# Kernel optimization log

Hardware: AMD Instinct MI355X
Metric: run time of the kernel (lower is better)

## Reference

```python
import jax, jax.numpy as jnp
import numpy as np

B, S, D, H = 4, 2048, 256, 4
HD = D // H          # head_dim = 64
SPARSITY = 0.1
NH2 = H * H          # 16, distill feature size


def _linear_params(key, out_d, in_d):
    # torch nn.Linear default init: U(-1/sqrt(in), 1/sqrt(in)) for W and b
    limit = 1.0 / np.sqrt(in_d)
    kw, kb = jax.random.split(key)
    W = jax.random.uniform(kw, (out_d, in_d), minval=-limit, maxval=limit, dtype=jnp.float32)
    b = jax.random.uniform(kb, (out_d,), minval=-limit, maxval=limit, dtype=jnp.float32)
    return W, b


def setup_inputs() -> dict:
    key = jax.random.key(0)
    ks = jax.random.split(key, 8)
    x = jax.random.normal(ks[0], (B, S, D), dtype=jnp.float32)
    Wq, bq = _linear_params(ks[1], D, D)
    Wk, bk = _linear_params(ks[2], D, D)
    Wv, bv = _linear_params(ks[3], D, D)
    Wd, bd = _linear_params(ks[4], NH2, NH2)      # distill: 16 -> 16
    Wg, bg = _linear_params(ks[5], NH2, D)        # gate: dim -> 16 (then sigmoid)
    Wgp, bgp = _linear_params(ks[6], D, NH2)      # gate_projection: 16 -> dim
    Wo, bo = _linear_params(ks[7], D, D)          # out: dim -> dim
    return dict(x=x, Wq=Wq, bq=bq, Wk=Wk, bk=bk, Wv=Wv, bv=bv,
                Wd=Wd, bd=bd, Wg=Wg, bg=bg, Wgp=Wgp, bgp=bgp, Wo=Wo, bo=bo)


def reference(x, Wq, bq, Wk, bk, Wv, bv, Wd, bd, Wg, bg, Wgp, bgp, Wo, bo):
    b, s, d = x.shape
    scale = HD ** -0.5
    # QKV projections, split into heads: [b, h, s, hd]
    Q = (x @ Wq.T + bq).reshape(b, s, H, HD).transpose(0, 2, 1, 3)
    K = (x @ Wk.T + bk).reshape(b, s, H, HD).transpose(0, 2, 1, 3)
    V = (x @ Wv.T + bv).reshape(b, s, H, HD).transpose(0, 2, 1, 3)
    scores = jnp.einsum('bhqd,bhkd->bhqk', Q, K) * scale  # [b,h,s,s]
    # per-row quantile threshold (torch.quantile linear interpolation == jnp default)
    q = 1.0 - SPARSITY  # 0.9
    thr = jnp.quantile(scores, q, axis=-1, keepdims=True)
    masked = jnp.where(scores >= thr, scores, -jnp.inf)
    probs = jax.nn.softmax(masked, axis=-1)
    att = jnp.einsum('bhqk,bhkd->bhqd', probs, V)
    att = att.transpose(0, 2, 1, 3).reshape(b, s, d)  # [b,s,dim]
    # distill: view as (-1, 16) -> Linear(16,16) -> view back
    distilled = (att.reshape(-1, NH2) @ Wd.T + bd).reshape(b, s, d)
    # gate from mean-pooled input
    g = jax.nn.sigmoid(x.mean(axis=1) @ Wg.T + bg)  # [b,16]
    g = (g @ Wgp.T + bgp)[:, None, :]               # [b,1,dim] broadcast over seq
    mixed = g * distilled + (1.0 - g) * att
    return mixed @ Wo.T + bo
```

## Files before the change

### kernel.cpp

```cpp
#include <hip/hip_runtime.h>
#include <hip/hip_bf16.h>
#include <math.h>


#define CAP 128

typedef __attribute__((ext_vector_type(8))) short short8;
typedef __attribute__((ext_vector_type(4))) float floatx4;
typedef _Float16 half8 __attribute__((ext_vector_type(8)));
typedef _Float16 half4v __attribute__((ext_vector_type(4)));
#define MFMA16(a,b,c) __builtin_amdgcn_mfma_f32_16x16x32_bf16(a,b,c,0,0,0)
#define MFMAH(a,b,c)  __builtin_amdgcn_mfma_f32_16x16x32_f16(a,b,c,0,0,0)

__device__ __forceinline__ float umt(unsigned u){
  return __uint_as_float((u & 0x80000000u) ? (u & 0x7fffffffu) : ~u);
}
__device__ __forceinline__ float wmin_f(float v){
  #pragma unroll
  for (int m=1;m<64;m<<=1) v = fminf(v, __shfl_xor(v,m,64));
  return v;
}
__device__ __forceinline__ int mbcnt64(unsigned long long m){
  return (int)__builtin_amdgcn_mbcnt_hi((unsigned)(m>>32),
         __builtin_amdgcn_mbcnt_lo((unsigned)(m & 0xffffffffull), 0u));
}
__device__ __forceinline__ short8 ldb8(const __hip_bfloat16* p){
  return *(const short8*)p;
}

#define FULLSEL(SU, PSTART, V206, V205)                                        \
  {                                                                            \
    unsigned v = (PSTART);                                                     \
    _Pragma("unroll 1")                                                        \
    for (int bit = 19; bit >= 0; --bit){                                       \
      const float cf = umt(v | (1u << bit));                                   \
      int n = 0;                                                               \
      _Pragma("unroll")                                                        \
      for (int i = 0; i < 32; i++) n += (int)__popcll(__ballot(SU[i] >= cf));  \
      if (n >= 206) v |= (1u << bit);                                          \
    }                                                                          \
    V206 = umt(v);                                                             \
    int cgt = 0; float mn = 3.0e38f;                                           \
    _Pragma("unroll")                                                          \
    for (int i = 0; i < 32; i++){                                              \
      const float u = SU[i];                                                   \
      const bool gt = (u > V206);                                              \
      cgt += (int)__popcll(__ballot(gt));                                      \
      mn = (gt && u < mn) ? u : mn;                                            \
    }                                                                          \
    mn = wmin_f(mn);                                                           \
    V205 = (cgt == 205) ? mn : V206;                                           \
  }

__global__ void xpart_kernel(const float* __restrict__ x, float* __restrict__ xpart){
  const int ch = blockIdx.x, b = blockIdx.y, t = threadIdx.x;
  const float* xp = x + ((size_t)b*2048 + (size_t)ch*128)*256 + t;
  float s = 0.f;
  for (int i=0;i<128;i++) s += xp[(size_t)i*256];
  xpart[(size_t)(b*16+ch)*256 + t] = s;
}

__global__ void gate_kernel(const float* __restrict__ xpart,
                            const float* __restrict__ Wg, const float* __restrict__ bg,
                            const float* __restrict__ Wgp,const float* __restrict__ bgp,
                            float* __restrict__ gate_ws){
  __shared__ float xm[256];
  __shared__ float g16[16];
  const int t = threadIdx.x;
  const int b = blockIdx.x;
  float s = 0.f;
  for (int ch=0; ch<16; ch++) s += xpart[(size_t)(b*16+ch)*256 + t];
  xm[t] = s * (1.0f/2048.0f);
  __syncthreads();
  if (t < 16){
    float z = bg[t];
    for (int d=0; d<256; d++) z = fmaf(xm[d], Wg[t*256+d], z);
    g16[t] = 1.0f/(1.0f + __expf(-z));
  }
  __syncthreads();
  float z2 = bgp[t];
  #pragma unroll
  for (int j=0;j<16;j++) z2 = fmaf(g16[j], Wgp[t*16+j], z2);
  gate_ws[b*256 + t] = z2;
}

__global__ __launch_bounds__(256) void qkv_gemm(
    const float* __restrict__ x,
    const float* __restrict__ Wq, const float* __restrict__ bq,
    const float* __restrict__ Wk, const float* __restrict__ bk,
    const float* __restrict__ Wv, const float* __restrict__ bv,
    __hip_bfloat16* __restrict__ qh, __hip_bfloat16* __restrict__ ql,
    __hip_bfloat16* __restrict__ kh, __hip_bfloat16* __restrict__ kl,
    _Float16* __restrict__ vth, _Float16* __restrict__ vtl){
  __shared__ float As[16][68];
  __shared__ float Bs[16][68];
  const int m0 = blockIdx.x * 64;
  const int n0g = blockIdx.y * 64;
  const int sect = n0g >> 8;
  const int nloc0 = n0g & 255;
  const float* W    = (sect==0) ? Wq : ((sect==1) ? Wk : Wv);
  const float* bias = (sect==0) ? bq : ((sect==1) ? bk : bv);
  const int tid = threadIdx.x;
  const int ty = tid >> 4, tx = tid & 15;
  const int lr = tid >> 2, lc = tid & 3;

  float c[4][4];
  #pragma unroll
  for (int i=0;i<4;i++){
    #pragma unroll
    for (int j=0;j<4;j++) c[i][j]=0.f;
  }

  for (int k0=0; k0<256; k0+=16){
    float4 av  = *(const float4*)&x[(size_t)(m0+lr)*256 + k0 + lc*4];
    float4 bv4 = *(const float4*)&W[(size_t)(nloc0+lr)*256 + k0 + lc*4];
    __syncthreads();
    As[lc*4+0][lr]=av.x;  As[lc*4+1][lr]=av.y;  As[lc*4+2][lr]=av.z;  As[lc*4+3][lr]=av.w;
    Bs[lc*4+0][lr]=bv4.x; Bs[lc*4+1][lr]=bv4.y; Bs[lc*4+2][lr]=bv4.z; Bs[lc*4+3][lr]=bv4.w;
    __syncthreads();
    #pragma unroll
    for (int kk=0; kk<16; kk++){
      float4 a  = *(const float4*)&As[kk][ty*4];
      float4 b4 = *(const float4*)&Bs[kk][tx*4];
      c[0][0]=fmaf(a.x,b4.x,c[0][0]); c[0][1]=fmaf(a.x,b4.y,c[0][1]); c[0][2]=fmaf(a.x,b4.z,c[0][2]); c[0][3]=fmaf(a.x,b4.w,c[0][3]);
      c[1][0]=fmaf(a.y,b4.x,c[1][0]); c[1][1]=fmaf(a.y,b4.y,c[1][1]); c[1][2]=fmaf(a.y,b4.z,c[1][2]); c[1][3]=fmaf(a.y,b4.w,c[1][3]);
      c[2][0]=fmaf(a.z,b4.x,c[2][0]); c[2][1]=fmaf(a.z,b4.y,c[2][1]); c[2][2]=fmaf(a.z,b4.z,c[2][2]); c[2][3]=fmaf(a.z,b4.w,c[2][3]);
      c[3][0]=fmaf(a.w,b4.x,c[3][0]); c[3][1]=fmaf(a.w,b4.y,c[3][1]); c[3][2]=fmaf(a.w,b4.z,c[3][2]); c[3][3]=fmaf(a.w,b4.w,c[3][3]);
    }
  }

  if (sect == 2){
    const int mB = m0 + ty*4;
    const int bidx = mB >> 11, s0 = mB & 2047;
    #pragma unroll
    for (int j=0;j<4;j++){
      const int f = nloc0 + tx*4 + j;
      const int hh = f >> 6, hd = f & 63;
      const float bf = bias[f];
      half4v hv, lv;
      #pragma unroll
      for (int i=0;i<4;i++){
        const float val = c[i][j] + bf;
        const _Float16 hx = (_Float16)val;
        hv[i] = hx;
        lv[i] = (_Float16)(val - (float)hx);
      }
      const size_t row = (size_t)((bidx*4+hh)*64 + hd);
      *(half4v*)(vth + row*2048 + s0) = hv;
      *(half4v*)(vtl + row*2048 + s0) = lv;
    }
  } else {
    #pragma unroll
    for (int i=0;i<4;i++){
      const int m = m0 + ty*4 + i;
      const int bidx = m >> 11, s = m & 2047;
      #pragma unroll
      for (int j=0;j<4;j++){
        const int f = nloc0 + tx*4 + j;
        const float val = c[i][j] + bias[f];
        const int hh = f >> 6, hd = f & 63;
        const size_t idx = (size_t)((bidx*4+hh)*2048 + s)*64 + hd;
        const __hip_bfloat16 hi = __float2bfloat16(val);
        const float lo = val - __bfloat162float(hi);
        if (sect == 0){ qh[idx] = hi; ql[idx] = __float2bfloat16(lo); }
        else          { kh[idx] = hi; kl[idx] = __float2bfloat16(lo); }
      }
    }
  }
}

__global__ __launch_bounds__(512, 4) void attn_kernel(
    const __hip_bfloat16* __restrict__ qh, const __hip_bfloat16* __restrict__ ql,
    const __hip_bfloat16* __restrict__ kh, const __hip_bfloat16* __restrict__ kl,
    const _Float16* __restrict__ vth, const _Float16* __restrict__ vtl,
    const float* __restrict__ Wd, const float* __restrict__ bd,
    const float* __restrict__ gate_ws, float* __restrict__ mix_ws){
  __shared__ __align__(16) char smem[74240];
  __shared__ float obuf[16][66];
  __shared__ float zbuf[16];

  float (*buf0)[516] = (float (*)[516])smem;
  float (*buf1)[516] = (float (*)[516])(smem + 33024);

  const int bh = blockIdx.y;
  const int q0 = blockIdx.x * 16;
  const int tid = threadIdx.x;
  const int w = tid >> 6, ln = tid & 63;
  const int lm = ln & 15;
  const int lk = (ln >> 4) * 8;
  const int qa = 2*w, qb = 2*w + 1;

  const __hip_bfloat16* Qh = qh + ((size_t)bh*2048 + q0)*64;
  const __hip_bfloat16* Ql = ql + ((size_t)bh*2048 + q0)*64;
  const __hip_bfloat16* Kh = kh + ((size_t)bh*2048 + w*256)*64;
  const __hip_bfloat16* Kl = kl + ((size_t)bh*2048 + w*256)*64;

  float su0[32], su1[32];

  const short8 ah0 = ldb8(Qh + lm*64 + lk);
  const short8 ah1 = ldb8(Qh + lm*64 + 32 + lk);
  const short8 al0 = ldb8(Ql + lm*64 + lk);
  const short8 al1 = ldb8(Ql + lm*64 + 32 + lk);

  #pragma unroll
  for (int c = 0; c < 4; c++){
    float (*bufc)[516] = (c & 1) ? buf1 : buf0;
    floatx4 acc[4];
    #pragma unroll
    for (int tl = 0; tl < 4; tl++){
      const int krow = c*64 + tl*16 + lm;
      short8 bh0 = ldb8(Kh + krow*64 + lk);
      short8 bh1 = ldb8(Kh + krow*64 + 32 + lk);
      short8 bl0 = ldb8(Kl + krow*64 + lk);
      short8 bl1 = ldb8(Kl + krow*64 + 32 + lk);
      floatx4 a = {0.f,0.f,0.f,0.f};
      a = MFMA16(ah0, bh0, a);
      a = MFMA16(ah1, bh1, a);
      a = MFMA16(al0, bh0, a);
      a = MFMA16(al1, bh1, a);
      a = MFMA16(ah0, bl0, a);
      a = MFMA16(ah1, bl1, a);
      a = MFMA16(al0, bl0, a);
      a = MFMA16(al1, bl1, a);
      acc[tl] = a;
    }
    const int wr = (ln >> 4) * 4;
    #pragma unroll
    for (int tl = 0; tl < 4; tl++){
      const int col = w*64 + tl*16 + lm;
      bufc[wr+0][col] = acc[tl].x * 0.125f;
      bufc[wr+1][col] = acc[tl].y * 0.125f;
      bufc[wr+2][col] = acc[tl].z * 0.125f;
      bufc[wr+3][col] = acc[tl].w * 0.125f;
    }
    __syncthreads();
    float4 ra0 = *(const float4*)&bufc[qa][4*ln];
    float4 ra1 = *(const float4*)&bufc[qa][256 + 4*ln];
    float4 rb0 = *(const float4*)&bufc[qb][4*ln];
    float4 rb1 = *(const float4*)&bufc[qb][256 + 4*ln];
    const int o = c*8;
    su0[o+0]=ra0.x; su0[o+1]=ra0.y; su0[o+2]=ra0.z; su0[o+3]=ra0.w;
    su0[o+4]=ra1.x; su0[o+5]=ra1.y; su0[o+6]=ra1.z; su0[o+7]=ra1.w;
    su1[o+0]=rb0.x; su1[o+1]=rb0.y; su1[o+2]=rb0.z; su1[o+3]=rb0.w;
    su1[o+4]=rb1.x; su1[o+5]=rb1.y; su1[o+6]=rb1.z; su1[o+7]=rb1.w;
  }
  __syncthreads();

  unsigned p0 = 0, p1 = 0;
  #pragma unroll 1
  for (int bit = 31; bit >= 20; --bit){
    const float c0f = umt(p0 | (1u << bit));
    const float c1f = umt(p1 | (1u << bit));
    int v0 = 0, n1 = 0;
    #pragma unroll
    for (int i = 0; i < 32; i++){
      v0 += (su0[i] >= c0f) ? 1 : 0;
      n1 += (int)__popcll(__ballot(su1[i] >= c1f));
    }
    #pragma unroll
    for (int m=1;m<64;m<<=1) v0 += __shfl_xor(v0,m,64);
    p0 |= (v0 >= 206) ? (1u << bit) : 0u;
    if (n1 >= 206) p1 |= (1u << bit);
  }

  const int b = bh >> 2, h = bh & 3;

  const float pf0  = umt(p0),             pf1  = umt(p1);
  const float hif0 = umt(p0 + 0x100000u), hif1 = umt(p1 + 0x100000u);
  float* cand0 = (float*)(smem + 65536 + (size_t)(2*w + 0)*512);
  float* cand1 = (float*)(smem + 65536 + (size_t)(2*w + 1)*512);

  int above0 = 0, nc0 = 0, above1 = 0, nc1 = 0;
  float mx0 = -3.0e38f, mx1 = -3.0e38f, mnab0 = 3.0e38f, mnab1 = 3.0e38f;
  #pragma unroll
  for (int i = 0; i < 32; i++){
    const float u0 = su0[i], u1 = su1[i];
    mx0 = fmaxf(mx0, u0);
    mx1 = fmaxf(mx1, u1);
    const bool ab0 = (u0 >= hif0), ab1 = (u1 >= hif1);
    above0 += ab0 ? 1 : 0;
    above1 += ab1 ? 1 : 0;
    if (ab0) mnab0 = fminf(mnab0, u0);
    if (ab1) mnab1 = fminf(mnab1, u1);
    const bool cd0 = (u0 >= pf0) && !ab0, cd1 = (u1 >= pf1) && !ab1;
    const unsigned long long bal0 = __ballot(cd0);
    if (cd0){
      const int pos = nc0 + mbcnt64(bal0);
      if (pos < CAP) cand0[pos] = u0;
    }
    nc0 += (int)__popcll(bal0);
    const unsigned long long bal1 = __ballot(cd1);
    if (cd1){
      const int pos = nc1 + mbcnt64(bal1);
      if (pos < CAP) cand1[pos] = u1;
    }
    nc1 += (int)__popcll(bal1);
  }
  int ab01 = above0 | (above1 << 16);
  #pragma unroll
  for (int m=1;m<64;m<<=1){
    ab01  += __shfl_xor(ab01, m,64);
    mx0   = fmaxf(mx0,   __shfl_xor(mx0,  m,64));
    mx1   = fmaxf(mx1,   __shfl_xor(mx1,  m,64));
    mnab0 = fminf(mnab0, __shfl_xor(mnab0,m,64));
    mnab1 = fminf(mnab1, __shfl_xor(mnab1,m,64));
  }
  above0 = ab01 & 0xffff;
  above1 = ab01 >> 16;

  float v206_0, v205_0, v206_1, v205_1;
  if (__builtin_expect(nc0 <= CAP && nc1 <= CAP, 1)){
    const int j0 = 206 - above0, j1 = 206 - above1;
    const float cv00 = (ln      < nc0) ? cand0[ln]      : -3.0e38f;
    const float cv01 = (ln + 64 < nc0) ? cand0[ln + 64] : -3.0e38f;
    const float cv10 = (ln      < nc1) ? cand1[ln]      : -3.0e38f;
    const float cv11 = (ln + 64 < nc1) ? cand1[ln + 64] : -3.0e38f;
    unsigned v0 = p0, v1 = p1;
    #pragma unroll 1
    for (int bit = 19; bit >= 0; --bit){
      const float cf0 = umt(v0 | (1u << bit));
      const float cf1 = umt(v1 | (1u << bit));
      const int n0 = (int)__popcll(__ballot(cv00 >= cf0))
                   + (int)__popcll(__ballot(cv01 >= cf0));
      const int n1 = (int)__popcll(__ballot(cv10 >= cf1))
                   + (int)__popcll(__ballot(cv11 >= cf1));
      if (n0 >= j0) v0 |= (1u << bit);
      if (n1 >= j1) v1 |= (1u << bit);
    }
    v206_0 = umt(v0);
    v206_1 = umt(v1);
    const int cgtc0 = (int)__popcll(__ballot(cv00 > v206_0))
                    + (int)__popcll(__ballot(cv01 > v206_0));
    const int cgtc1 = (int)__popcll(__ballot(cv10 > v206_1))
                    + (int)__popcll(__ballot(cv11 > v206_1));
    float mnc0 = 3.0e38f, mnc1 = 3.0e38f;
    if (cv00 > v206_0) mnc0 = fminf(mnc0, cv00);
    if (cv01 > v206_0) mnc0 = fminf(mnc0, cv01);
    if (cv10 > v206_1) mnc1 = fminf(mnc1, cv10);
    if (cv11 > v206_1) mnc1 = fminf(mnc1, cv11);
    #pragma unroll
    for (int m=1;m<64;m<<=1){
      mnc0 = fminf(mnc0, __shfl_xor(mnc0,m,64));
      mnc1 = fminf(mnc1, __shfl_xor(mnc1,m,64));
    }
    const int cgt0 = above0 + cgtc0, cgt1 = above1 + cgtc1;
    v205_0 = (cgt0 == 205) ? ((cgtc0 > 0) ? mnc0 : mnab0) : v206_0;
    v205_1 = (cgt1 == 205) ? ((cgtc1 > 0) ? mnc1 : mnab1) : v206_1;
  } else {
    FULLSEL(su0, p0, v206_0, v205_0);
    FULLSEL(su1, p1, v206_1, v205_1);
  }

  const float thr0 = (float)((double)v206_0 + 0.3*((double)v205_0 - (double)v206_0));
  const float thr1 = (float)((double)v206_1 + 0.3*((double)v205_1 - (double)v206_1));

  float zl0 = 0.f, zl1 = 0.f;
  char* rba = smem + (size_t)qa*4096 + ((size_t)(ln >> 4) << 9)
            + (size_t)((((ln & 15) << 3)) ^ ((qa & 7) << 4));
  char* rbb = smem + (size_t)qb*4096 + ((size_t)(ln >> 4) << 9)
            + (size_t)((((ln & 15) << 3)) ^ ((qb & 7) << 4));
  #pragma unroll
  for (int c = 0; c < 4; c++){
    #pragma unroll
    for (int h4 = 0; h4 < 2; h4++){
      half4v pk0, pk1;
      #pragma unroll
      for (int jj = 0; jj < 4; jj++){
        const int i = c*8 + h4*4 + jj;
        const float s0 = su0[i], s1 = su1[i];
        const float pr0 = (s0 >= thr0) ? __expf(s0 - mx0) : 0.f;
        const float pr1 = (s1 >= thr1) ? __expf(s1 - mx1) : 0.f;
        const _Float16 ph0 = (_Float16)pr0;
        const _Float16 ph1 = (_Float16)pr1;
        zl0 += (float)ph0;
        zl1 += (float)ph1;
        pk0[jj] = ph0;
        pk1[jj] = ph1;
      }
      *(half4v*)(rba + h4*2048 + c*128) = pk0;
      *(half4v*)(rbb + h4*2048 + c*128) = pk1;
    }
  }
  #pragma unroll
  for (int m=1;m<64;m<<=1){
    zl0 += __shfl_xor(zl0,m,64);
    zl1 += __shfl_xor(zl1,m,64);
  }
  if (ln == 0){ zbuf[qa] = 1.0f / zl0; zbuf[qb] = 1.0f / zl1; }

  __syncthreads();

  const int ct = w & 3, kh2 = w >> 2;
  const int arow = ln & 15;
  const int sw = (arow & 7) << 4;
  const char* prow = smem + (size_t)arow*4096;
  const int klog0 = (kh2 << 11) + ((ln >> 4) << 4);
  const _Float16* vhp = vth + ((size_t)bh*64 + ct*16 + arow)*2048 + (kh2 << 10) + ((ln >> 4) << 3);
  const _Float16* vlp = vtl + ((size_t)bh*64 + ct*16 + arow)*2048 + (kh2 << 10) + ((ln >> 4) << 3);

  floatx4 acch = {0.f,0.f,0.f,0.f};
  floatx4 accl = {0.f,0.f,0.f,0.f};
  #pragma unroll 4
  for (int kk = 0; kk < 32; kk++){
    const half8 a   = *(const half8*)(prow + ((klog0 + kk*64) ^ sw));
    const half8 vh8 = *(const half8*)(vhp + kk*32);
    const half8 vl8 = *(const half8*)(vlp + kk*32);
    acch = MFMAH(a, vh8, acch);
    accl = MFMAH(a, vl8, accl);
  }
  floatx4 acc = acch + accl;

  float gt = 0.f, bda = 0.f;
  float wdv[16];
  if (kh2 == 1){
    const int r0 = (ln >> 4) * 4;
    #pragma unroll
    for (int i = 0; i < 4; i++) obuf[r0+i][ct*16 + arow] = acc[i];
  } else {
    gt  = gate_ws[(size_t)b*256 + h*64 + ct*16 + arow];
    bda = bd[arow];
    #pragma unroll
    for (int m4 = 0; m4 < 4; m4++){
      const float4 t4 = *(const float4*)&Wd[arow*16 + m4*4];
      wdv[m4*4+0]=t4.x; wdv[m4*4+1]=t4.y; wdv[m4*4+2]=t4.z; wdv[m4*4+3]=t4.w;
    }
  }
  __syncthreads();
  if (kh2 == 0){
    const int r0 = (ln >> 4) * 4;
    const int gb = ln & 48;
    #pragma unroll
    for (int i = 0; i < 4; i++){
      const int r = r0 + i;
      const float o = (acc[i] + obuf[r][ct*16 + arow]) * zbuf[r];
      float d = bda;
      #pragma unroll
      for (int m = 0; m < 16; m++)
        d = fmaf(__shfl(o, gb + m, 64), wdv[m], d);
      const float mixed = gt*d + (1.0f - gt)*o;
      mix_ws[(size_t)(b*2048 + q0 + r)*256 + h*64 + ct*16 + arow] = mixed;
    }
  }
}

__global__ __launch_bounds__(256) void out_gemm(
    const float* __restrict__ A, const float* __restrict__ Wo,
    const float* __restrict__ bo, float* __restrict__ out){
  __shared__ float As[16][68];
  __shared__ float Bs[16][68];
  const int m0 = blockIdx.x * 64;
  const int n0 = blockIdx.y * 64;
  const int tid = threadIdx.x;
  const int ty = tid >> 4, tx = tid & 15;
  const int lr = tid >> 2, lc = tid & 3;

  float c[4][4];
  #pragma unroll
  for (int i=0;i<4;i++){
    #pragma unroll
    for (int j=0;j<4;j++) c[i][j]=0.f;
  }

  for (int k0=0; k0<256; k0+=16){
    float4 av  = *(const float4*)&A[(size_t)(m0+lr)*256 + k0 + lc*4];
    float4 bv4 = *(const float4*)&Wo[(size_t)(n0+lr)*256 + k0 + lc*4];
    __syncthreads();
    As[lc*4+0][lr]=av.x;  As[lc*4+1][lr]=av.y;  As[lc*4+2][lr]=av.z;  As[lc*4+3][lr]=av.w;
    Bs[lc*4+0][lr]=bv4.x; Bs[lc*4+1][lr]=bv4.y; Bs[lc*4+2][lr]=bv4.z; Bs[lc*4+3][lr]=bv4.w;
    __syncthreads();
    #pragma unroll
    for (int kk=0; kk<16; kk++){
      float4 a  = *(const float4*)&As[kk][ty*4];
      float4 b4 = *(const float4*)&Bs[kk][tx*4];
      c[0][0]=fmaf(a.x,b4.x,c[0][0]); c[0][1]=fmaf(a.x,b4.y,c[0][1]); c[0][2]=fmaf(a.x,b4.z,c[0][2]); c[0][3]=fmaf(a.x,b4.w,c[0][3]);
      c[1][0]=fmaf(a.y,b4.x,c[1][0]); c[1][1]=fmaf(a.y,b4.y,c[1][1]); c[1][2]=fmaf(a.y,b4.z,c[1][2]); c[1][3]=fmaf(a.y,b4.w,c[1][3]);
      c[2][0]=fmaf(a.z,b4.x,c[2][0]); c[2][1]=fmaf(a.z,b4.y,c[2][1]); c[2][2]=fmaf(a.z,b4.z,c[2][2]); c[2][3]=fmaf(a.z,b4.w,c[2][3]);
      c[3][0]=fmaf(a.w,b4.x,c[3][0]); c[3][1]=fmaf(a.w,b4.y,c[3][1]); c[3][2]=fmaf(a.w,b4.z,c[3][2]); c[3][3]=fmaf(a.w,b4.w,c[3][3]);
    }
  }
  #pragma unroll
  for (int i=0;i<4;i++){
    const int m = m0 + ty*4 + i;
    float4 st = make_float4(c[i][0]+bo[n0+tx*4+0], c[i][1]+bo[n0+tx*4+1],
                            c[i][2]+bo[n0+tx*4+2], c[i][3]+bo[n0+tx*4+3]);
    *(float4*)&out[(size_t)m*256 + n0 + tx*4] = st;
  }
}

extern "C" void kernel_launch(void* const* d_in, const int* in_sizes, int n_in,
                              void* d_out, int out_size, void* d_ws, size_t ws_size,
                              hipStream_t stream) {
  const float* x   = (const float*)d_in[0];
  const float* Wq  = (const float*)d_in[1];  const float* bq  = (const float*)d_in[2];
  const float* Wk  = (const float*)d_in[3];  const float* bk  = (const float*)d_in[4];
  const float* Wv  = (const float*)d_in[5];  const float* bv  = (const float*)d_in[6];
  const float* Wd  = (const float*)d_in[7];  const float* bd  = (const float*)d_in[8];
  const float* Wg  = (const float*)d_in[9];  const float* bg  = (const float*)d_in[10];
  const float* Wgp = (const float*)d_in[11]; const float* bgp = (const float*)d_in[12];
  const float* Wo  = (const float*)d_in[13]; const float* bo  = (const float*)d_in[14];

  char* base = (char*)d_ws;
  float* mix_ws = (float*)(base);
  __hip_bfloat16* qh = (__hip_bfloat16*)(base + (size_t)( 8<<20));
  __hip_bfloat16* ql = (__hip_bfloat16*)(base + (size_t)(12<<20));
  __hip_bfloat16* kh = (__hip_bfloat16*)(base + (size_t)(16<<20));
  __hip_bfloat16* kl = (__hip_bfloat16*)(base + (size_t)(20<<20));
  _Float16* vth = (_Float16*)(base + (size_t)(24<<20));
  _Float16* vtl = (_Float16*)(base + (size_t)(28<<20));
  float* xpart  = (float*)(base + (size_t)(32<<20));
  float* gate_ws= (float*)(base + (size_t)(32<<20) + 65536);

  xpart_kernel<<<dim3(16,4), 256, 0, stream>>>(x, xpart);
  gate_kernel<<<4, 256, 0, stream>>>(xpart, Wg, bg, Wgp, bgp, gate_ws);
  qkv_gemm<<<dim3(128,12), 256, 0, stream>>>(x, Wq,bq, Wk,bk, Wv,bv, qh,ql,kh,kl, vth,vtl);
  attn_kernel<<<dim3(128,16), 512, 0, stream>>>(qh, ql, kh, kl, vth, vtl,
                                                Wd, bd, gate_ws, mix_ws);
  out_gemm<<<dim3(128,4), 256, 0, stream>>>(mix_ws, Wo, bo, (float*)d_out);
}
```

Before: 438.8 us.

## Move QKV and output projections to split-bf16 MFMA GEMMs

Replaces the FP32 SIMT shared-memory GEMMs for the QKV and output projections with bf16 MFMA 16x16x32 kernels. They use a hi/lo split (three-term products plus lo*lo) to keep near-FP32 accuracy. Inputs x and the weight matrices are pre-split into bf16 hi/lo buffers by the xpart kernel and a new weight-conversion kernel. The attention kernel now writes its mixed output as hi/lo bf16 as well. This trades an extra launch and extra workspace traffic for matrix-core throughput in the projection GEMMs.

```diff
diff --git a/kernel.cpp b/kernel.cpp
--- a/kernel.cpp
+++ b/kernel.cpp
@@ -52,12 +52,42 @@
     V205 = (cgt == 205) ? mn : V206;                                           \
   }
 
-__global__ void xpart_kernel(const float* __restrict__ x, float* __restrict__ xpart){
+__global__ void xpart_kernel(const float* __restrict__ x, float* __restrict__ xpart,
+                             __hip_bfloat16* __restrict__ xh, __hip_bfloat16* __restrict__ xl){
   const int ch = blockIdx.x, b = blockIdx.y, t = threadIdx.x;
-  const float* xp = x + ((size_t)b*2048 + (size_t)ch*128)*256 + t;
+  const size_t base = ((size_t)b*2048 + (size_t)ch*128)*256 + t;
   float s = 0.f;
-  for (int i=0;i<128;i++) s += xp[(size_t)i*256];
+  for (int i=0;i<128;i++){
+    const float v = x[base + (size_t)i*256];
+    s += v;
+    const __hip_bfloat16 h = __float2bfloat16(v);
+    xh[base + (size_t)i*256] = h;
+    xl[base + (size_t)i*256] = __float2bfloat16(v - __bfloat162float(h));
+  }
   xpart[(size_t)(b*16+ch)*256 + t] = s;
+}
+
+__global__ void wconv_kernel(const float* __restrict__ Wq, const float* __restrict__ Wk,
+                             const float* __restrict__ Wv, const float* __restrict__ Wo,
+                             __hip_bfloat16* __restrict__ wh, __hip_bfloat16* __restrict__ wl){
+  const int mat = blockIdx.x >> 6;
+  const float* W = (mat==0) ? Wq : (mat==1) ? Wk : (mat==2) ? Wv : Wo;
+  const int off = (blockIdx.x & 63)*1024 + threadIdx.x*4;
+  const float4 v = *(const float4*)&W[off];
+  short4 h4, l4;
+  const float vv[4] = {v.x, v.y, v.z, v.w};
+  short hs[4], ls[4];
+  #pragma unroll
+  for (int i=0;i<4;i++){
+    const __hip_bfloat16 h = __float2bfloat16(vv[i]);
+    const __hip_bfloat16 l = __float2bfloat16(vv[i] - __bfloat162float(h));
+    hs[i] = *(const short*)&h; ls[i] = *(const short*)&l;
+  }
+  h4 = make_short4(hs[0],hs[1],hs[2],hs[3]);
+  l4 = make_short4(ls[0],ls[1],ls[2],ls[3]);
+  const size_t o = (size_t)mat*65536 + off;
+  *(short4*)((short*)wh + o) = h4;
+  *(short4*)((short*)wl + o) = l4;
 }
 
 __global__ void gate_kernel(const float* __restrict__ xpart,
@@ -85,62 +115,55 @@
 }
 
 __global__ __launch_bounds__(256) void qkv_gemm(
-    const float* __restrict__ x,
-    const float* __restrict__ Wq, const float* __restrict__ bq,
-    const float* __restrict__ Wk, const float* __restrict__ bk,
-    const float* __restrict__ Wv, const float* __restrict__ bv,
+    const __hip_bfloat16* __restrict__ xh, const __hip_bfloat16* __restrict__ xl,
+    const __hip_bfloat16* __restrict__ wh, const __hip_bfloat16* __restrict__ wl,
+    const float* __restrict__ bq, const float* __restrict__ bk, const float* __restrict__ bv,
     __hip_bfloat16* __restrict__ qh, __hip_bfloat16* __restrict__ ql,
     __hip_bfloat16* __restrict__ kh, __hip_bfloat16* __restrict__ kl,
     _Float16* __restrict__ vth, _Float16* __restrict__ vtl){
-  __shared__ float As[16][68];
-  __shared__ float Bs[16][68];
   const int m0 = blockIdx.x * 64;
   const int n0g = blockIdx.y * 64;
   const int sect = n0g >> 8;
-  const int nloc0 = n0g & 255;
-  const float* W    = (sect==0) ? Wq : ((sect==1) ? Wk : Wv);
+  const int nl0 = n0g & 255;
+  const __hip_bfloat16* Bh = wh + (size_t)sect*65536;
+  const __hip_bfloat16* Bl = wl + (size_t)sect*65536;
   const float* bias = (sect==0) ? bq : ((sect==1) ? bk : bv);
   const int tid = threadIdx.x;
-  const int ty = tid >> 4, tx = tid & 15;
-  const int lr = tid >> 2, lc = tid & 3;
-
-  float c[4][4];
-  #pragma unroll
-  for (int i=0;i<4;i++){
-    #pragma unroll
-    for (int j=0;j<4;j++) c[i][j]=0.f;
-  }
-
-  for (int k0=0; k0<256; k0+=16){
-    float4 av  = *(const float4*)&x[(size_t)(m0+lr)*256 + k0 + lc*4];
-    float4 bv4 = *(const float4*)&W[(size_t)(nloc0+lr)*256 + k0 + lc*4];
-    __syncthreads();
-    As[lc*4+0][lr]=av.x;  As[lc*4+1][lr]=av.y;  As[lc*4+2][lr]=av.z;  As[lc*4+3][lr]=av.w;
-    Bs[lc*4+0][lr]=bv4.x; Bs[lc*4+1][lr]=bv4.y; Bs[lc*4+2][lr]=bv4.z; Bs[lc*4+3][lr]=bv4.w;
-    __syncthreads();
-    #pragma unroll
-    for (int kk=0; kk<16; kk++){
-      float4 a  = *(const float4*)&As[kk][ty*4];
-      float4 b4 = *(const float4*)&Bs[kk][tx*4];
-      c[0][0]=fmaf(a.x,b4.x,c[0][0]); c[0][1]=fmaf(a.x,b4.y,c[0][1]); c[0][2]=fmaf(a.x,b4.z,c[0][2]); c[0][3]=fmaf(a.x,b4.w,c[0][3]);
-      c[1][0]=fmaf(a.y,b4.x,c[1][0]); c[1][1]=fmaf(a.y,b4.y,c[1][1]); c[1][2]=fmaf(a.y,b4.z,c[1][2]); c[1][3]=fmaf(a.y,b4.w,c[1][3]);
-      c[2][0]=fmaf(a.z,b4.x,c[2][0]); c[2][1]=fmaf(a.z,b4.y,c[2][1]); c[2][2]=fmaf(a.z,b4.z,c[2][2]); c[2][3]=fmaf(a.z,b4.w,c[2][3]);
-      c[3][0]=fmaf(a.w,b4.x,c[3][0]); c[3][1]=fmaf(a.w,b4.y,c[3][1]); c[3][2]=fmaf(a.w,b4.z,c[3][2]); c[3][3]=fmaf(a.w,b4.w,c[3][3]);
-    }
-  }
-
-  if (sect == 2){
-    const int mB = m0 + ty*4;
-    const int bidx = mB >> 11, s0 = mB & 2047;
-    #pragma unroll
-    for (int j=0;j<4;j++){
-      const int f = nloc0 + tx*4 + j;
-      const int hh = f >> 6, hd = f & 63;
-      const float bf = bias[f];
+  const int w = tid >> 6, ln = tid & 63;
+  const int lm = ln & 15, lk = (ln >> 4) * 8;
+  const int arow = m0 + w*16 + lm;
+
+  floatx4 acc[4];
+  #pragma unroll
+  for (int tl=0;tl<4;tl++) acc[tl] = (floatx4){0.f,0.f,0.f,0.f};
+
+  for (int k0 = 0; k0 < 256; k0 += 32){
+    const short8 ah = ldb8(xh + (size_t)arow*256 + k0 + lk);
+    const short8 al = ldb8(xl + (size_t)arow*256 + k0 + lk);
+    #pragma unroll
+    for (int tl = 0; tl < 4; tl++){
+      const int bcol = nl0 + tl*16 + lm;
+      const short8 bh8 = ldb8(Bh + (size_t)bcol*256 + k0 + lk);
+      const short8 bl8 = ldb8(Bl + (size_t)bcol*256 + k0 + lk);
+      acc[tl] = MFMA16(ah, bh8, acc[tl]);
+      acc[tl] = MFMA16(al, bh8, acc[tl]);
+      acc[tl] = MFMA16(ah, bl8, acc[tl]);
+      acc[tl] = MFMA16(al, bl8, acc[tl]);
+    }
+  }
+
+  #pragma unroll
+  for (int tl = 0; tl < 4; tl++){
+    const int f = nl0 + tl*16 + lm;
+    const int hh = f >> 6, hd = f & 63;
+    const float bf = bias[f];
+    if (sect == 2){
+      const int mB = m0 + w*16 + (ln >> 4)*4;
+      const int bidx = mB >> 11, s0 = mB & 2047;
       half4v hv, lv;
       #pragma unroll
       for (int i=0;i<4;i++){
-        const float val = c[i][j] + bf;
+        const float val = acc[tl][i] + bf;
         const _Float16 hx = (_Float16)val;
         hv[i] = hx;
         lv[i] = (_Float16)(val - (float)hx);
@@ -148,17 +171,12 @@
       const size_t row = (size_t)((bidx*4+hh)*64 + hd);
       *(half4v*)(vth + row*2048 + s0) = hv;
       *(half4v*)(vtl + row*2048 + s0) = lv;
-    }
-  } else {
-    #pragma unroll
-    for (int i=0;i<4;i++){
-      const int m = m0 + ty*4 + i;
-      const int bidx = m >> 11, s = m & 2047;
+    } else {
       #pragma unroll
-      for (int j=0;j<4;j++){
-        const int f = nloc0 + tx*4 + j;
-        const float val = c[i][j] + bias[f];
-        const int hh = f >> 6, hd = f & 63;
+      for (int i=0;i<4;i++){
+        const int m = m0 + w*16 + (ln >> 4)*4 + i;
+        const int bidx = m >> 11, s = m & 2047;
+        const float val = acc[tl][i] + bf;
         const size_t idx = (size_t)((bidx*4+hh)*2048 + s)*64 + hd;
         const __hip_bfloat16 hi = __float2bfloat16(val);
         const float lo = val - __bfloat162float(hi);
@@ -174,7 +192,8 @@
     const __hip_bfloat16* __restrict__ kh, const __hip_bfloat16* __restrict__ kl,
     const _Float16* __restrict__ vth, const _Float16* __restrict__ vtl,
     const float* __restrict__ Wd, const float* __restrict__ bd,
-    const float* __restrict__ gate_ws, float* __restrict__ mix_ws){
+    const float* __restrict__ gate_ws,
+    __hip_bfloat16* __restrict__ mixh, __hip_bfloat16* __restrict__ mixl){
   __shared__ __align__(16) char smem[74240];
   __shared__ float obuf[16][66];
   __shared__ float zbuf[16];
@@ -438,52 +457,55 @@
       for (int m = 0; m < 16; m++)
         d = fmaf(__shfl(o, gb + m, 64), wdv[m], d);
       const float mixed = gt*d + (1.0f - gt)*o;
-      mix_ws[(size_t)(b*2048 + q0 + r)*256 + h*64 + ct*16 + arow] = mixed;
+      const size_t oidx = (size_t)(b*2048 + q0 + r)*256 + h*64 + ct*16 + arow;
+      const __hip_bfloat16 mhv = __float2bfloat16(mixed);
+      mixh[oidx] = mhv;
+      mixl[oidx] = __float2bfloat16(mixed - __bfloat162float(mhv));
     }
   }
 }
 
 __global__ __launch_bounds__(256) void out_gemm(
-    const float* __restrict__ A, const float* __restrict__ Wo,
+    const __hip_bfloat16* __restrict__ mh, const __hip_bfloat16* __restrict__ ml,
+    const __hip_bfloat16* __restrict__ wh, const __hip_bfloat16* __restrict__ wl,
     const float* __restrict__ bo, float* __restrict__ out){
-  __shared__ float As[16][68];
-  __shared__ float Bs[16][68];
   const int m0 = blockIdx.x * 64;
   const int n0 = blockIdx.y * 64;
+  const __hip_bfloat16* Bh = wh + (size_t)3*65536;
+  const __hip_bfloat16* Bl = wl + (size_t)3*65536;
   const int tid = threadIdx.x;
-  const int ty = tid >> 4, tx = tid & 15;
-  const int lr = tid >> 2, lc = tid & 3;
-
-  float c[4][4];
-  #pragma unroll
-  for (int i=0;i<4;i++){
-    #pragma unroll
-    for (int j=0;j<4;j++) c[i][j]=0.f;
-  }
-
-  for (int k0=0; k0<256; k0+=16){
-    float4 av  = *(const float4*)&A[(size_t)(m0+lr)*256 + k0 + lc*4];
-    float4 bv4 = *(const float4*)&Wo[(size_t)(n0+lr)*256 + k0 + lc*4];
-    __syncthreads();
-    As[lc*4+0][lr]=av.x;  As[lc*4+1][lr]=av.y;  As[lc*4+2][lr]=av.z;  As[lc*4+3][lr]=av.w;
-    Bs[lc*4+0][lr]=bv4.x; Bs[lc*4+1][lr]=bv4.y; Bs[lc*4+2][lr]=bv4.z; Bs[lc*4+3][lr]=bv4.w;
-    __syncthreads();
-    #pragma unroll
-    for (int kk=0; kk<16; kk++){
-      float4 a  = *(const float4*)&As[kk][ty*4];
-      float4 b4 = *(const float4*)&Bs[kk][tx*4];
-      c[0][0]=fmaf(a.x,b4.x,c[0][0]); c[0][1]=fmaf(a.x,b4.y,c[0][1]); c[0][2]=fmaf(a.x,b4.z,c[0][2]); c[0][3]=fmaf(a.x,b4.w,c[0][3]);
-      c[1][0]=fmaf(a.y,b4.x,c[1][0]); c[1][1]=fmaf(a.y,b4.y,c[1][1]); c[1][2]=fmaf(a.y,b4.z,c[1][2]); c[1][3]=fmaf(a.y,b4.w,c[1][3]);
-      c[2][0]=fmaf(a.z,b4.x,c[2][0]); c[2][1]=fmaf(a.z,b4.y,c[2][1]); c[2][2]=fmaf(a.z,b4.z,c[2][2]); c[2][3]=fmaf(a.z,b4.w,c[2][3]);
-      c[3][0]=fmaf(a.w,b4.x,c[3][0]); c[3][1]=fmaf(a.w,b4.y,c[3][1]); c[3][2]=fmaf(a.w,b4.z,c[3][2]); c[3][3]=fmaf(a.w,b4.w,c[3][3]);
-    }
-  }
-  #pragma unroll
-  for (int i=0;i<4;i++){
-    const int m = m0 + ty*4 + i;
-    float4 st = make_float4(c[i][0]+bo[n0+tx*4+0], c[i][1]+bo[n0+tx*4+1],
-                            c[i][2]+bo[n0+tx*4+2], c[i][3]+bo[n0+tx*4+3]);
-    *(float4*)&out[(size_t)m*256 + n0 + tx*4] = st;
+  const int w = tid >> 6, ln = tid & 63;
+  const int lm = ln & 15, lk = (ln >> 4) * 8;
+  const int arow = m0 + w*16 + lm;
+
+  floatx4 acc[4];
+  #pragma unroll
+  for (int tl=0;tl<4;tl++) acc[tl] = (floatx4){0.f,0.f,0.f,0.f};
+
+  for (int k0 = 0; k0 < 256; k0 += 32){
+    const short8 ah = ldb8(mh + (size_t)arow*256 + k0 + lk);
+    const short8 al = ldb8(ml + (size_t)arow*256 + k0 + lk);
+    #pragma unroll
+    for (int tl = 0; tl < 4; tl++){
+      const int bcol = n0 + tl*16 + lm;
+      const short8 bh8 = ldb8(Bh + (size_t)bcol*256 + k0 + lk);
+      const short8 bl8 = ldb8(Bl + (size_t)bcol*256 + k0 + lk);
+      acc[tl] = MFMA16(ah, bh8, acc[tl]);
+      acc[tl] = MFMA16(al, bh8, acc[tl]);
+      acc[tl] = MFMA16(ah, bl8, acc[tl]);
+      acc[tl] = MFMA16(al, bl8, acc[tl]);
+    }
+  }
+
+  #pragma unroll
+  for (int tl = 0; tl < 4; tl++){
+    const int f = n0 + tl*16 + lm;
+    const float bf = bo[f];
+    #pragma unroll
+    for (int i=0;i<4;i++){
+      const int m = m0 + w*16 + (ln >> 4)*4 + i;
+      out[(size_t)m*256 + f] = acc[tl][i] + bf;
+    }
   }
 }
 
@@ -500,20 +522,27 @@
   const float* Wo  = (const float*)d_in[13]; const float* bo  = (const float*)d_in[14];
 
   char* base = (char*)d_ws;
-  float* mix_ws = (float*)(base);
+  __hip_bfloat16* mixh = (__hip_bfloat16*)(base);
+  __hip_bfloat16* mixl = (__hip_bfloat16*)(base + (size_t)( 4<<20));
   __hip_bfloat16* qh = (__hip_bfloat16*)(base + (size_t)( 8<<20));
   __hip_bfloat16* ql = (__hip_bfloat16*)(base + (size_t)(12<<20));
   __hip_bfloat16* kh = (__hip_bfloat16*)(base + (size_t)(16<<20));
   __hip_bfloat16* kl = (__hip_bfloat16*)(base + (size_t)(20<<20));
   _Float16* vth = (_Float16*)(base + (size_t)(24<<20));
   _Float16* vtl = (_Float16*)(base + (size_t)(28<<20));
-  float* xpart  = (float*)(base + (size_t)(32<<20));
-  float* gate_ws= (float*)(base + (size_t)(32<<20) + 65536);
-
-  xpart_kernel<<<dim3(16,4), 256, 0, stream>>>(x, xpart);
+  __hip_bfloat16* xh = (__hip_bfloat16*)(base + (size_t)(32<<20));
+  __hip_bfloat16* xl = (__hip_bfloat16*)(base + (size_t)(36<<20));
+  __hip_bfloat16* wh = (__hip_bfloat16*)(base + (size_t)(40<<20));
+  __hip_bfloat16* wl = (__hip_bfloat16*)(base + (size_t)(40<<20) + (512<<10));
+  float* xpart  = (float*)(base + (size_t)(41<<20));
+  float* gate_ws= (float*)(base + (size_t)(41<<20) + 65536);
+
+  xpart_kernel<<<dim3(16,4), 256, 0, stream>>>(x, xpart, xh, xl);
+  wconv_kernel<<<256, 256, 0, stream>>>(Wq, Wk, Wv, Wo, wh, wl);
   gate_kernel<<<4, 256, 0, stream>>>(xpart, Wg, bg, Wgp, bgp, gate_ws);
-  qkv_gemm<<<dim3(128,12), 256, 0, stream>>>(x, Wq,bq, Wk,bk, Wv,bv, qh,ql,kh,kl, vth,vtl);
+  qkv_gemm<<<dim3(128,12), 256, 0, stream>>>(xh, xl, wh, wl, bq, bk, bv,
+                                             qh, ql, kh, kl, vth, vtl);
   attn_kernel<<<dim3(128,16), 512, 0, stream>>>(qh, ql, kh, kl, vth, vtl,
-                                                Wd, bd, gate_ws, mix_ws);
-  out_gemm<<<dim3(128,4), 256, 0, stream>>>(mix_ws, Wo, bo, (float*)d_out);
-}
+                                                Wd, bd, gate_ws, mixh, mixl);
+  out_gemm<<<dim3(128,4), 256, 0, stream>>>(mixh, mixl, wh, wl, bo, (float*)d_out);
+}
```

After: 472.6 us. 7.7% more time.
